# Kernel tuning notes

Measured on AMD Instinct MI355X. Metric: run time of the kernel, lower is better.

Reference implementation:

```python
import jax, jax.numpy as jnp
import numpy as np

ALPHA = 0.2          # LeakyReLU negative slope
NEG = -9e15          # masking value from the torch source


def _gat_multihead(x, adj, W, a):
    """All nheads GATLayers (concat=True math, elu applied by caller).
    x: [B,N,F], adj: [B,N,N], W: [H,F,O], a: [H,2O]. Returns [B,H,N,O].
    Note a_input @ a decomposes as h_i.a[:O] + h_j.a[O:], so we never
    materialize the O(N^2 * 2O) pairwise concat tensor."""
    h = jnp.einsum('bnf,hfo->bhno', x, W)            # [B,H,N,O]
    O = h.shape[-1]
    s1 = jnp.einsum('bhno,ho->bhn', h, a[:, :O])     # h_i . a_src
    s2 = jnp.einsum('bhno,ho->bhn', h, a[:, O:])     # h_j . a_dst
    e = jax.nn.leaky_relu(s1[..., :, None] + s2[..., None, :], ALPHA)  # [B,H,N,N]
    att = jax.nn.softmax(jnp.where(adj[:, None] > 0, e, NEG), axis=-1)
    return jnp.einsum('bhij,bhjo->bhio', att, h)


def _gat_single(x, adj, W, a):
    """out_att GATLayer (concat=False, no elu). W: [F,O], a: [2O]."""
    h = jnp.einsum('bnf,fo->bno', x, W)
    O = W.shape[-1]
    s1 = h @ a[:O]
    s2 = h @ a[O:]
    e = jax.nn.leaky_relu(s1[:, :, None] + s2[:, None, :], ALPHA)
    att = jax.nn.softmax(jnp.where(adj > 0, e, NEG), axis=-1)
    return jnp.einsum('bij,bjo->bio', att, h)


def setup_inputs() -> dict:
    key = jax.random.key(0)
    ks = jax.random.split(key, 10)
    B, N, F = 2, 2048, 768
    H, O = 8, 256
    x = jax.random.normal(ks[0], (B, N, F), dtype=jnp.float32)
    # sparse-ish binary adjacency (adj>0 is all that matters) + self loops
    adj = (jax.random.uniform(ks[1], (B, N, N)) < 0.05).astype(jnp.float32)
    adj = jnp.maximum(adj, jnp.eye(N, dtype=jnp.float32)[None])
    mask = jnp.ones((B, N, 1), dtype=jnp.float32)  # unused by GAT.forward
    s = 0.05
    W_heads = jax.random.normal(ks[2], (H, F, O), dtype=jnp.float32) * s
    a_heads = jax.random.normal(ks[3], (H, 2 * O), dtype=jnp.float32) * s
    W_out = jax.random.normal(ks[4], (H * O, O), dtype=jnp.float32) * s
    a_out = jax.random.normal(ks[5], (2 * O,), dtype=jnp.float32) * s
    W_lin = jax.random.normal(ks[6], (O, H * O), dtype=jnp.float32) * s  # nn.Linear weight [out,in]
    b_lin = jnp.zeros((O,), dtype=jnp.float32)
    W_ln = jax.random.normal(ks[7], (O, O), dtype=jnp.float32) * s
    b_ln = jnp.zeros((O,), dtype=jnp.float32)
    return {"x": x, "adj": adj, "mask": mask, "W_heads": W_heads,
            "a_heads": a_heads, "W_out": W_out, "a_out": a_out,
            "W_lin": W_lin, "b_lin": b_lin, "W_ln": W_ln, "b_ln": b_ln}


def reference(x, adj, mask, W_heads, a_heads, W_out, a_out, W_lin, b_lin, W_ln, b_ln):
    # layer 0: multi-head GAT, elu, concat over heads (dropout=0 in eval)
    hp = jax.nn.elu(_gat_multihead(x, adj, W_heads, a_heads))  # [B,H,N,O]
    B, H, N, O = hp.shape
    x1 = jnp.transpose(hp, (0, 2, 1, 3)).reshape(B, N, H * O)
    # layer 1: residual linear + out_att (concat=False)
    x2 = x1 @ W_lin.T + b_lin + _gat_single(x1, adj, W_out, a_out)
    # final: relu(ln(x))
    return jax.nn.relu(x2 @ W_ln.T + b_ln)
```

## Files before the change

kernel.cpp:

```cpp
#include <hip/hip_runtime.h>
#include <hip/hip_bf16.h>

constexpr int Bb = 2, Nn = 2048, Ff = 768, Hh = 8, Oo = 256;

typedef __attribute__((ext_vector_type(8)))  short   short8;
typedef __attribute__((ext_vector_type(16))) float   f32x16;
typedef __attribute__((ext_vector_type(4)))  unsigned short ushort4_t;

__device__ inline unsigned short f2bf(float f) {
    unsigned u = __float_as_uint(f);
    u = (u + 0x7FFFu + ((u >> 16) & 1u)) >> 16;
    return (unsigned short)u;
}

__device__ inline void wfrag_kn_body(
        const float* __restrict__ W, unsigned short* __restrict__ out,
        int K, int N, int fblk, int t) {
    int f = fblk * 4 + (t >> 6);
    int slot = t & 63, kh = slot >> 5, lm = slot & 31;
    int nfk = K >> 4;
    int nt = f / nfk, kt = f - nt * nfk;
    const float* wp = W + (size_t)(kt * 16 + kh * 8) * N + nt * 32 + lm;
    ushort4_t o0, o1;
    o0.x = f2bf(wp[0]);             o0.y = f2bf(wp[(size_t)N]);
    o0.z = f2bf(wp[2 * (size_t)N]); o0.w = f2bf(wp[3 * (size_t)N]);
    o1.x = f2bf(wp[4 * (size_t)N]); o1.y = f2bf(wp[5 * (size_t)N]);
    o1.z = f2bf(wp[6 * (size_t)N]); o1.w = f2bf(wp[7 * (size_t)N]);
    unsigned short* op = out + (size_t)f * 512 + slot * 8;
    *(ushort4_t*)op = o0;
    *(ushort4_t*)(op + 4) = o1;
}

__device__ inline void wfrag_nk_body(
        const float* __restrict__ W, unsigned short* __restrict__ out,
        int K, int fblk, int t) {
    int f = fblk * 4 + (t >> 6);
    int slot = t & 63, kh = slot >> 5, lm = slot & 31;
    int nfk = K >> 4;
    int nt = f / nfk, kt = f - nt * nfk;
    const float* wp = W + (size_t)(nt * 32 + lm) * K + kt * 16 + kh * 8;
    float4 a = *(const float4*)wp, b = *(const float4*)(wp + 4);
    ushort4_t o0, o1;
    o0.x = f2bf(a.x); o0.y = f2bf(a.y); o0.z = f2bf(a.z); o0.w = f2bf(a.w);
    o1.x = f2bf(b.x); o1.y = f2bf(b.y); o1.z = f2bf(b.z); o1.w = f2bf(b.w);
    unsigned short* op = out + (size_t)f * 512 + slot * 8;
    *(ushort4_t*)op = o0;
    *(ushort4_t*)(op + 4) = o1;
}

__global__ __launch_bounds__(256) void prep_misc_kernel(
        const float* __restrict__ adj, unsigned long long* __restrict__ bits,
        const float* __restrict__ x, unsigned short* __restrict__ x_bf,
        const float* __restrict__ W_heads, unsigned short* __restrict__ WhF,
        const float* __restrict__ W_out,   unsigned short* __restrict__ WoF,
        const float* __restrict__ W_lin,   unsigned short* __restrict__ WlF,
        const float* __restrict__ W_ln,    unsigned short* __restrict__ WnF) {
    int blk = blockIdx.x, t = threadIdx.x;
    if (blk < 32768) {
        size_t gid = (size_t)blk * 256 + t;
        float v = adj[gid];
        unsigned long long m = __ballot(v > 0.f);
        if ((t & 63) == 0) bits[gid >> 6] = m;
    } else if (blk < 35840) {
        size_t i = (size_t)(blk - 32768) * 256 + t;
        float4 v = ((const float4*)x)[i];
        ushort4_t o;
        o.x = f2bf(v.x); o.y = f2bf(v.y); o.z = f2bf(v.z); o.w = f2bf(v.w);
        ((ushort4_t*)x_bf)[i] = o;
    } else if (blk < 36608) {
        int idx = blk - 35840;
        int head = idx / 96, fblk = idx - head * 96;
        wfrag_kn_body(W_heads + (size_t)head * Ff * Oo, WhF + (size_t)head * 384 * 512,
                      Ff, Oo, fblk, t);
    } else if (blk < 36864) {
        wfrag_kn_body(W_out, WoF, Hh * Oo, Oo, blk - 36608, t);
    } else if (blk < 37120) {
        wfrag_nk_body(W_lin, WlF, Hh * Oo, blk - 36864, t);
    } else {
        wfrag_nk_body(W_ln, WnF, Oo, blk - 37120, t);
    }
}

template<int SWAPZ>
__global__ __launch_bounds__(256) void gemm32_kernel(
        const unsigned short* __restrict__ A, int K, long long sA, int bAshift,
        const unsigned short* __restrict__ BF, long long sB, int bmask,
        float* __restrict__ C, long long sC,
        unsigned short* __restrict__ CF, long long sCF, int Mtot,
        const float* __restrict__ bias, int mode,
        const float* __restrict__ aall, int amask,
        float* __restrict__ E1p, float* __restrict__ E1n, float2* __restrict__ E2pn) {
    int z  = SWAPZ ? blockIdx.x : blockIdx.z;
    int mx = SWAPZ ? blockIdx.y : blockIdx.x;
    A  += (size_t)(z >> bAshift) * sA;
    BF += (size_t)(z & bmask) * sB;
    if (C) C += (size_t)z * sC;
    if (CF) CF += (size_t)z * sCF;
    int m0 = mx * 32;
    int t = threadIdx.x;
    int wv = t >> 6, lane = t & 63;
    int lm = lane & 31, kh = lane >> 5;
    int nfk = K >> 4;
    __shared__ __align__(16) unsigned short As[32][136];
    f32x16 acc[2] = {};
    int sr = t >> 3, sc2 = (t & 7) * 16;
    const unsigned short* ag  = A + (size_t)(m0 + sr) * K + sc2;
    const unsigned short* bg0 = BF + (size_t)(wv * 2) * nfk * 512;
    const unsigned short* bg1 = bg0 + (size_t)nfk * 512;
    for (int k0 = 0; k0 < K; k0 += 128) {
        *(short8*)&As[sr][sc2]     = *(const short8*)(ag + k0);
        *(short8*)&As[sr][sc2 + 8] = *(const short8*)(ag + k0 + 8);
        int kt0 = k0 >> 4;
        __syncthreads();
#pragma unroll
        for (int s = 0; s < 8; ++s) {
            short8 a0 = *(const short8*)&As[lm][s * 16 + kh * 8];
            short8 b0 = *(const short8*)(bg0 + (size_t)(kt0 + s) * 512 + lane * 8);
            short8 b1 = *(const short8*)(bg1 + (size_t)(kt0 + s) * 512 + lane * 8);
            acc[0] = __builtin_amdgcn_mfma_f32_32x32x16_bf16(a0, b0, acc[0], 0, 0, 0);
            acc[1] = __builtin_amdgcn_mfma_f32_32x32x16_bf16(a0, b1, acc[1], 0, 0, 0);
        }
        __syncthreads();
    }
#pragma unroll
    for (int nt = 0; nt < 2; ++nt) {
        int colg = wv * 64 + nt * 32 + lm;
        float bv = (mode == 2) ? bias[colg] : 0.f;
        if (C) {
#pragma unroll
            for (int reg = 0; reg < 16; ++reg) {
                int rl = 4 * kh + (reg & 3) + 8 * (reg >> 2);
                float v = acc[nt][reg];
                if (mode == 2) { v += bv; v = fmaxf(v, 0.f); }
                C[(size_t)(m0 + rl) * 256 + colg] = v;
            }
        }
        if (mode == 1) {
#pragma unroll
            for (int q = 0; q < 4; ++q) {
                int kt = m0 / 16 + (q >> 1);
                size_t fi = ((size_t)(colg >> 5) * (Mtot / 16) + kt) * 512 +
                            ((q & 1) * 32 + (colg & 31)) * 8 + kh * 4;
                ushort4_t pk;
                pk.x = f2bf(acc[nt][q * 4 + 0]);
                pk.y = f2bf(acc[nt][q * 4 + 1]);
                pk.z = f2bf(acc[nt][q * 4 + 2]);
                pk.w = f2bf(acc[nt][q * 4 + 3]);
                *(ushort4_t*)(CF + fi) = pk;
            }
        }
    }
    if (aall) {
        const float* av = aall + (size_t)(z & amask) * 512;
        float a1v0 = av[wv * 64 + lm],       a1v1 = av[wv * 64 + 32 + lm];
        float a2v0 = av[256 + wv * 64 + lm], a2v1 = av[256 + wv * 64 + 32 + lm];
        float* sbuf = (float*)As;
#pragma unroll
        for (int reg = 0; reg < 16; ++reg) {
            int rl = 4 * kh + (reg & 3) + 8 * (reg >> 2);
            float v1 = acc[0][reg] * a1v0 + acc[1][reg] * a1v1;
            float v2 = acc[0][reg] * a2v0 + acc[1][reg] * a2v1;
#pragma unroll
            for (int m = 1; m <= 16; m <<= 1) {
                v1 += __shfl_xor(v1, m, 64);
                v2 += __shfl_xor(v2, m, 64);
            }
            if (lm == 0) { sbuf[rl * 8 + wv] = v1; sbuf[rl * 8 + 4 + wv] = v2; }
        }
        __syncthreads();
        if (t < 32) {
            float s1 = sbuf[t * 8] + sbuf[t * 8 + 1] + sbuf[t * 8 + 2] + sbuf[t * 8 + 3];
            float s2 = sbuf[t * 8 + 4] + sbuf[t * 8 + 5] + sbuf[t * 8 + 6] + sbuf[t * 8 + 7];
            size_t ei = (size_t)z * Nn + m0 + t;
            E1p[ei] = __expf(s1);
            E1n[ei] = __expf(0.2f * s1);
            E2pn[ei] = make_float2(__expf(s2), __expf(0.2f * s2));
        }
    }
}

__global__ __launch_bounds__(512) void gemm32_dual_kernel(
        const unsigned short* __restrict__ A, int K, long long sA,
        const unsigned short* __restrict__ BF,
        unsigned short* __restrict__ h2f, float* __restrict__ lin,
        const float* __restrict__ a_out,
        float* __restrict__ E1p, float* __restrict__ E1n, float2* __restrict__ E2pn) {
    int b = blockIdx.z, ng = blockIdx.y;
    A += (size_t)b * sA;
    int nfk = K >> 4;
    BF += (size_t)ng * 8 * nfk * 512;
    int m0 = blockIdx.x * 32;
    int t = threadIdx.x;
    int wv = t >> 6, lane = t & 63;
    int lm = lane & 31, kh = lane >> 5;
    __shared__ __align__(16) unsigned short As[32][136];
    f32x16 acc = {};
    int sr = t >> 4, sc2 = (t & 15) * 8;
    const unsigned short* ag = A + (size_t)(m0 + sr) * K + sc2;
    const unsigned short* bg = BF + (size_t)wv * nfk * 512;
    for (int k0 = 0; k0 < K; k0 += 128) {
        *(short8*)&As[sr][sc2] = *(const short8*)(ag + k0);
        int kt0 = k0 >> 4;
        __syncthreads();
#pragma unroll
        for (int s = 0; s < 8; ++s) {
            short8 a0 = *(const short8*)&As[lm][s * 16 + kh * 8];
            short8 b0 = *(const short8*)(bg + (size_t)(kt0 + s) * 512 + lane * 8);
            acc = __builtin_amdgcn_mfma_f32_32x32x16_bf16(a0, b0, acc, 0, 0, 0);
        }
        __syncthreads();
    }
    int colg = wv * 32 + lm;
    if (ng == 1) {
        float* C = lin + (size_t)b * Nn * 256;
#pragma unroll
        for (int reg = 0; reg < 16; ++reg) {
            int rl = 4 * kh + (reg & 3) + 8 * (reg >> 2);
            C[(size_t)(m0 + rl) * 256 + colg] = acc[reg];
        }
    } else {
        unsigned short* CF = h2f + (size_t)b * 524288;
#pragma unroll
        for (int q = 0; q < 4; ++q) {
            int kt = m0 / 16 + (q >> 1);
            size_t fi = ((size_t)(colg >> 5) * 128 + kt) * 512 +
                        ((q & 1) * 32 + (colg & 31)) * 8 + kh * 4;
            ushort4_t pk;
            pk.x = f2bf(acc[q * 4 + 0]);
            pk.y = f2bf(acc[q * 4 + 1]);
            pk.z = f2bf(acc[q * 4 + 2]);
            pk.w = f2bf(acc[q * 4 + 3]);
            *(ushort4_t*)(CF + fi) = pk;
        }
        float a1v = a_out[colg];
        float a2v = a_out[256 + colg];
        float* sbuf = (float*)As;
#pragma unroll
        for (int reg = 0; reg < 16; ++reg) {
            int rl = 4 * kh + (reg & 3) + 8 * (reg >> 2);
            float v1 = acc[reg] * a1v;
            float v2 = acc[reg] * a2v;
#pragma unroll
            for (int m = 1; m <= 16; m <<= 1) {
                v1 += __shfl_xor(v1, m, 64);
                v2 += __shfl_xor(v2, m, 64);
            }
            if (lm == 0) { sbuf[rl * 16 + wv] = v1; sbuf[rl * 16 + 8 + wv] = v2; }
        }
        __syncthreads();
        if (t < 32) {
            float s1 = 0.f, s2 = 0.f;
#pragma unroll
            for (int k = 0; k < 8; ++k) {
                s1 += sbuf[t * 16 + k];
                s2 += sbuf[t * 16 + 8 + k];
            }
            size_t ei = (size_t)b * Nn + m0 + t;
            E1p[ei] = __expf(s1);
            E1n[ei] = __expf(0.2f * s1);
            E2pn[ei] = make_float2(__expf(s2), __expf(0.2f * s2));
        }
    }
}

__global__ __launch_bounds__(256) void gemm32_final_kernel(
        const float* __restrict__ pacc, const float* __restrict__ plsum,
        const float* __restrict__ lin, const float* __restrict__ b_lin,
        const unsigned short* __restrict__ BF, const float* __restrict__ b_ln,
        float* __restrict__ out) {
    int b = blockIdx.z, oc = blockIdx.y;
    int m0 = blockIdx.x * 32;
    int t = threadIdx.x;
    int wv = t >> 6, lane = t & 63;
    int lm = lane & 31, kh = lane >> 5;
    constexpr int nfk = 16;
    __shared__ __align__(16) unsigned short As[32][136];
    f32x16 acc = {};
    int sr = t >> 3, sc2 = (t & 7) * 16;
    int row = m0 + sr;
    int BN = Bb * Nn;
    size_t prow = (size_t)b * Nn + row;
    float li = 1.f / (plsum[prow] + plsum[prow + BN] + plsum[prow + 2 * BN] + plsum[prow + 3 * BN]);
    size_t ps4 = (size_t)Bb * Nn * 256;
    const unsigned short* bg = BF + (size_t)(oc * 4 + wv) * nfk * 512;
    for (int k0 = 0; k0 < 256; k0 += 128) {
        int o = k0 + sc2;
        size_t pidx = prow * 256 + o;
#pragma unroll
        for (int g = 0; g < 4; ++g) {
            float4 s4 = *(const float4*)(pacc + pidx + 4 * g);
#pragma unroll
            for (int k = 1; k < 4; ++k) {
                float4 q = *(const float4*)(pacc + k * ps4 + pidx + 4 * g);
                s4.x += q.x; s4.y += q.y; s4.z += q.z; s4.w += q.w;
            }
            float4 lv = *(const float4*)(lin + pidx + 4 * g);
            float4 bv = *(const float4*)(b_lin + o + 4 * g);
            ushort4_t pk;
            pk.x = f2bf(s4.x * li + lv.x + bv.x);
            pk.y = f2bf(s4.y * li + lv.y + bv.y);
            pk.z = f2bf(s4.z * li + lv.z + bv.z);
            pk.w = f2bf(s4.w * li + lv.w + bv.w);
            *(ushort4_t*)&As[sr][sc2 + 4 * g] = pk;
        }
        int kt0 = k0 >> 4;
        __syncthreads();
#pragma unroll
        for (int s = 0; s < 8; ++s) {
            short8 a0 = *(const short8*)&As[lm][s * 16 + kh * 8];
            short8 b0 = *(const short8*)(bg + (size_t)(kt0 + s) * 512 + lane * 8);
            acc = __builtin_amdgcn_mfma_f32_32x32x16_bf16(a0, b0, acc, 0, 0, 0);
        }
        __syncthreads();
    }
    float* C = out + (size_t)b * Nn * 256;
    int colg = oc * 128 + wv * 32 + lm;
    float bv = b_ln[colg];
#pragma unroll
    for (int reg = 0; reg < 16; ++reg) {
        int rl = 4 * kh + (reg & 3) + 8 * (reg >> 2);
        float v = fmaxf(acc[reg] + bv, 0.f);
        C[(size_t)(m0 + rl) * 256 + colg] = v;
    }
}

template<int JLEN, int MODE, int SWAPXY>
__global__ __launch_bounds__(256, 4) void attn_v8_kernel(
        const unsigned short* __restrict__ hfrag,
        const unsigned* __restrict__ bits,
        const float* __restrict__ E1p, const float* __restrict__ E1n,
        const float2* __restrict__ E2pn,
        unsigned short* __restrict__ outbf, int ldo,
        float* __restrict__ pacc, float* __restrict__ plsum,
        int hshift) {
    constexpr int W = JLEN / 32, NC = JLEN / 64, ABS = W + 1;
    int it = SWAPXY ? blockIdx.y : blockIdx.x;
    int bh = SWAPXY ? blockIdx.x : blockIdx.y;
    int js = blockIdx.z;
    int b = bh >> hshift, hd = bh & ((1 << hshift) - 1);
    int i0 = it * 32, jbase = js * JLEN;
    int kt0 = js * (JLEN / 16);
    int t = threadIdx.x, lane = t & 63;
    int wv = t >> 6, lm = lane & 31, kh = lane >> 5;
    int ti = t & 31, jq = t >> 5;

    __shared__ unsigned ab[32 * ABS];
    __shared__ __align__(16) unsigned short ps[2][32][64];
    __shared__ float lred[32][9];
    __shared__ float linv[32];

    const unsigned* bb = bits + ((size_t)b * Nn + i0) * 64 + (jbase >> 5);
    for (int k = t; k < 32 * W; k += 256) {
        int r = k / W, w0 = k - r * W;
        ab[r * ABS + w0] = bb[(size_t)r * 64 + w0];
    }
    __syncthreads();

    float e1p = E1p[(size_t)bh * Nn + i0 + ti];
    float e1n = E1n[(size_t)bh * Nn + i0 + ti];
    const float4* e2base = (const float4*)(E2pn + (size_t)bh * Nn + jbase);

    const unsigned short* bg0 = hfrag + (size_t)bh * 524288 + (size_t)(wv * 2) * 128 * 512;
    const unsigned short* bg1 = bg0 + 128 * 512;

    f32x16 acc[2] = {};
    float lp0 = 0.f, lp1 = 0.f;
    short8 Bpp[4][2];

    auto loadBs = [&](int c, int s, int slot) {
        int kt = kt0 + c * 4 + s;
        Bpp[slot][0] = *(const short8*)(bg0 + (size_t)kt * 512 + lane * 8);
        Bpp[slot][1] = *(const short8*)(bg1 + (size_t)kt * 512 + lane * 8);
    };
    auto computeP = [&](int c, int buf) {
        int cj = c * 64;
        unsigned word = ab[ti * ABS + (cj >> 5) + (jq >> 2)];
        unsigned field = (word >> ((jq & 3) * 8)) & 0xffu;
        const float4* ep = e2base + ((cj + jq * 8) >> 1);
        unsigned pk[4];
#pragma unroll
        for (int u = 0; u < 4; ++u) {
            float4 q = ep[u];
            float p0 = fmaxf(e1p * q.x, e1n * q.y);
            p0 = ((field >> (2 * u)) & 1u) ? p0 : 0.f;
            float p1 = fmaxf(e1p * q.z, e1n * q.w);
            p1 = ((field >> (2 * u + 1)) & 1u) ? p1 : 0.f;
            if (u & 1) lp1 += p0 + p1; else lp0 += p0 + p1;
            __hip_bfloat162 hv = __float22bfloat162_rn(make_float2(p0, p1));
            pk[u] = *(unsigned*)&hv;
        }
        uint4 v; v.x = pk[0]; v.y = pk[1]; v.z = pk[2]; v.w = pk[3];
        *(uint4*)&ps[buf][ti][(jq ^ (ti & 7)) * 8] = v;
    };
    auto mfmaS = [&](int buf, int s, int slot) {
        int g = 2 * s + kh;
        short8 a0 = *(const short8*)&ps[buf][lm][(g ^ (lm & 7)) * 8];
        __builtin_amdgcn_s_setprio(1);
        acc[0] = __builtin_amdgcn_mfma_f32_32x32x16_bf16(a0, Bpp[slot][0], acc[0], 0, 0, 0);
        acc[1] = __builtin_amdgcn_mfma_f32_32x32x16_bf16(a0, Bpp[slot][1], acc[1], 0, 0, 0);
        __builtin_amdgcn_s_setprio(0);
    };

    computeP(0, 0);
    loadBs(0, 0, 0); loadBs(0, 1, 1); loadBs(0, 2, 2); loadBs(0, 3, 3);
    __syncthreads();
    for (int c = 0; c + 1 < NC; ++c) {
        int cb = c & 1, nb = cb ^ 1;
        computeP(c + 1, nb);
        mfmaS(cb, 0, 0);  loadBs(c + 1, 0, 0);
        mfmaS(cb, 1, 1);  loadBs(c + 1, 1, 1);
        mfmaS(cb, 2, 2);  loadBs(c + 1, 2, 2);
        mfmaS(cb, 3, 3);  loadBs(c + 1, 3, 3);
        __syncthreads();
    }
    {
        int cb = (NC - 1) & 1;
        mfmaS(cb, 0, 0);
        mfmaS(cb, 1, 1);
        mfmaS(cb, 2, 2);
        mfmaS(cb, 3, 3);
    }

    lred[ti][jq] = lp0 + lp1;
    __syncthreads();
    if (MODE == 0) {
        if (t < 32) {
            float s = 0.f;
#pragma unroll
            for (int k = 0; k < 8; ++k) s += lred[t][k];
            linv[t] = 1.f / s;
        }
        __syncthreads();
#pragma unroll
        for (int nt = 0; nt < 2; ++nt) {
            int o = wv * 64 + nt * 32 + lm;
#pragma unroll
            for (int reg = 0; reg < 16; ++reg) {
                int rl = 4 * kh + (reg & 3) + 8 * (reg >> 2);
                float v = acc[nt][reg] * linv[rl];
                v = v > 0.f ? v : expm1f(v);
                outbf[((size_t)b * Nn + i0 + rl) * ldo + (size_t)hd * Oo + o] = f2bf(v);
            }
        }
    } else {
        if (t < 32) {
            float s = 0.f;
#pragma unroll
            for (int k = 0; k < 8; ++k) s += lred[t][k];
            plsum[((size_t)js * Bb + b) * Nn + i0 + t] = s;
        }
        float* pa = pacc + (((size_t)js * Bb + b) * Nn) * 256;
#pragma unroll
        for (int nt = 0; nt < 2; ++nt) {
            int o = wv * 64 + nt * 32 + lm;
#pragma unroll
            for (int reg = 0; reg < 16; ++reg) {
                int rl = 4 * kh + (reg & 3) + 8 * (reg >> 2);
                pa[(size_t)(i0 + rl) * 256 + o] = acc[nt][reg];
            }
        }
    }
}

extern "C" void kernel_launch(void* const* d_in, const int* in_sizes, int n_in,
                              void* d_out, int out_size, void* d_ws, size_t ws_size,
                              hipStream_t stream) {
    const float* x       = (const float*)d_in[0];
    const float* adj     = (const float*)d_in[1];
    const float* W_heads = (const float*)d_in[3];
    const float* a_heads = (const float*)d_in[4];
    const float* W_out   = (const float*)d_in[5];
    const float* a_out   = (const float*)d_in[6];
    const float* W_lin   = (const float*)d_in[7];
    const float* b_lin   = (const float*)d_in[8];
    const float* W_ln    = (const float*)d_in[9];
    const float* b_ln    = (const float*)d_in[10];

    char* w = (char*)d_ws;
    float* pacc     = (float*)(w);
    float* lin      = (float*)(w + 33554432);
    float* E1p_mh   = (float*)(w + 41943040);
    float* E1n_mh   = (float*)(w + 42074112);
    float2* E2pn_mh = (float2*)(w + 42205184);
    float* E1p_sh   = (float*)(w + 42467328);
    float* E1n_sh   = (float*)(w + 42483712);
    float2* E2pn_sh = (float2*)(w + 42500096);
    unsigned long long* bits = (unsigned long long*)(w + 42532864);
    unsigned short* x_bf  = (unsigned short*)(w + 43581440);
    unsigned short* WhF   = (unsigned short*)(w + 49872896);
    unsigned short* WoF   = (unsigned short*)(w + 53018624);
    unsigned short* WlF   = (unsigned short*)(w + 54067200);
    unsigned short* WnF   = (unsigned short*)(w + 55115776);
    unsigned short* hfrag = (unsigned short*)(w + 55246848);
    unsigned short* h2frag= (unsigned short*)(w + 72024064);
    unsigned short* x1_bf = (unsigned short*)(w + 74121216);
    float* plsum = E1p_mh;

    prep_misc_kernel<<<37152, 256, 0, stream>>>(
        adj, bits, x, x_bf, W_heads, WhF, W_out, WoF, W_lin, WlF, W_ln, WnF);

    gemm32_kernel<1><<<dim3(Bb * Hh, Nn / 32, 1), 256, 0, stream>>>(
        x_bf, Ff, (long long)Nn * Ff, 3, WhF, 384LL * 512, 7,
        nullptr, 0, hfrag, 524288, Nn, nullptr, 1,
        a_heads, 7, E1p_mh, E1n_mh, E2pn_mh);
    attn_v8_kernel<2048, 0, 1><<<dim3(Bb * Hh, Nn / 32, 1), 256, 0, stream>>>(
        hfrag, (const unsigned*)bits, E1p_mh, E1n_mh, E2pn_mh,
        x1_bf, Hh * Oo, nullptr, nullptr, 3);
    gemm32_dual_kernel<<<dim3(Nn / 32, 2, Bb), 512, 0, stream>>>(
        x1_bf, Hh * Oo, (long long)Nn * Hh * Oo, WoF, h2frag, lin,
        a_out, E1p_sh, E1n_sh, E2pn_sh);
    attn_v8_kernel<512, 1, 0><<<dim3(Nn / 32, Bb, 4), 256, 0, stream>>>(
        h2frag, (const unsigned*)bits, E1p_sh, E1n_sh, E2pn_sh,
        nullptr, 0, pacc, plsum, 0);
    gemm32_final_kernel<<<dim3(Nn / 32, 2, Bb), 256, 0, stream>>>(
        pacc, plsum, lin, b_lin, WnF, b_ln, (float*)d_out);
}
```

Measured before the change: 248.0 us.

## Restructure attention kernel to split K across waves with register-resident P fragments

The attention kernel now has each wave own a slice of the neighbour (K) dimension and compute all 256 output columns for it. Before, waves split the output columns and shared a P tile staged through double-buffered LDS. Each wave builds its P fragment directly in registers as the MFMA B-operand, which removes the per-chunk LDS round trip and the block barriers in the main loop. The partial sums from the four waves are combined through a 64KB LDS reduction in the epilogue, which then writes vectorised stores. The cost is eight accumulator tiles per wave, more registers, launch bounds lowered to 2 blocks per SIMD, and a larger LDS footprint that reduces occupancy.

```diff
diff --git a/kernel.cpp b/kernel.cpp
--- a/kernel.cpp
+++ b/kernel.cpp
@@ -325,7 +325,7 @@
 }
 
 template<int JLEN, int MODE, int SWAPXY>
-__global__ __launch_bounds__(256, 4) void attn_v8_kernel(
+__global__ __launch_bounds__(256, 2) void attn_v10_kernel(
         const unsigned short* __restrict__ hfrag,
         const unsigned* __restrict__ bits,
         const float* __restrict__ E1p, const float* __restrict__ E1n,
@@ -333,130 +333,137 @@
         unsigned short* __restrict__ outbf, int ldo,
         float* __restrict__ pacc, float* __restrict__ plsum,
         int hshift) {
-    constexpr int W = JLEN / 32, NC = JLEN / 64, ABS = W + 1;
+    constexpr int W = JLEN / 32;
+    constexpr int NC = JLEN / 64;
     int it = SWAPXY ? blockIdx.y : blockIdx.x;
     int bh = SWAPXY ? blockIdx.x : blockIdx.y;
     int js = blockIdx.z;
     int b = bh >> hshift, hd = bh & ((1 << hshift) - 1);
     int i0 = it * 32, jbase = js * JLEN;
     int kt0 = js * (JLEN / 16);
-    int t = threadIdx.x, lane = t & 63;
-    int wv = t >> 6, lm = lane & 31, kh = lane >> 5;
-    int ti = t & 31, jq = t >> 5;
-
-    __shared__ unsigned ab[32 * ABS];
-    __shared__ __align__(16) unsigned short ps[2][32][64];
-    __shared__ float lred[32][9];
-    __shared__ float linv[32];
+    int t = threadIdx.x;
+    int wv = t >> 6, lane = t & 63;
+    int lm = lane & 31, kh = lane >> 5;
+    int jq = wv * 2 + kh;
+
+    __shared__ __align__(16) char smem[65536 + 512];
+    float4*   epi4 = (float4*)smem;
+    unsigned* ab   = (unsigned*)smem;
+    float*    lred = (float*)(smem + 65536);
 
     const unsigned* bb = bits + ((size_t)b * Nn + i0) * 64 + (jbase >> 5);
     for (int k = t; k < 32 * W; k += 256) {
         int r = k / W, w0 = k - r * W;
-        ab[r * ABS + w0] = bb[(size_t)r * 64 + w0];
+        ab[r * W + w0] = bb[(size_t)r * 64 + w0];
     }
     __syncthreads();
 
-    float e1p = E1p[(size_t)bh * Nn + i0 + ti];
-    float e1n = E1n[(size_t)bh * Nn + i0 + ti];
+    float e1p = E1p[(size_t)bh * Nn + i0 + lm];
+    float e1n = E1n[(size_t)bh * Nn + i0 + lm];
     const float4* e2base = (const float4*)(E2pn + (size_t)bh * Nn + jbase);
-
-    const unsigned short* bg0 = hfrag + (size_t)bh * 524288 + (size_t)(wv * 2) * 128 * 512;
-    const unsigned short* bg1 = bg0 + 128 * 512;
-
-    f32x16 acc[2] = {};
+    const unsigned short* ag = hfrag + (size_t)bh * 524288 + lane * 8;
+
+    f32x16 acc[8] = {};
+    short8 A[8];
+    float4 e2a[4], e2b[4];
     float lp0 = 0.f, lp1 = 0.f;
-    short8 Bpp[4][2];
-
-    auto loadBs = [&](int c, int s, int slot) {
-        int kt = kt0 + c * 4 + s;
-        Bpp[slot][0] = *(const short8*)(bg0 + (size_t)kt * 512 + lane * 8);
-        Bpp[slot][1] = *(const short8*)(bg1 + (size_t)kt * 512 + lane * 8);
+
+    auto loadA = [&](int cn, int mt) {
+        int kt = kt0 + cn * 4 + wv;
+        A[mt] = *(const short8*)(ag + ((size_t)mt * 128 + kt) * 512);
     };
-    auto computeP = [&](int c, int buf) {
-        int cj = c * 64;
-        unsigned word = ab[ti * ABS + (cj >> 5) + (jq >> 2)];
+    auto loadE2 = [&](int cn, float4 (&buf)[4]) {
+        const float4* ep = e2base + ((cn * 64 + jq * 8) >> 1);
+#pragma unroll
+        for (int u = 0; u < 4; ++u) buf[u] = ep[u];
+    };
+    auto computeP = [&](int c, const float4 (&buf)[4], short8& pbo) {
+        unsigned word = ab[lm * W + c * 2 + (jq >> 2)];
         unsigned field = (word >> ((jq & 3) * 8)) & 0xffu;
-        const float4* ep = e2base + ((cj + jq * 8) >> 1);
-        unsigned pk[4];
+        union { unsigned u[4]; short8 s; } pk;
 #pragma unroll
         for (int u = 0; u < 4; ++u) {
-            float4 q = ep[u];
+            float4 q = buf[u];
             float p0 = fmaxf(e1p * q.x, e1n * q.y);
             p0 = ((field >> (2 * u)) & 1u) ? p0 : 0.f;
             float p1 = fmaxf(e1p * q.z, e1n * q.w);
             p1 = ((field >> (2 * u + 1)) & 1u) ? p1 : 0.f;
-            if (u & 1) lp1 += p0 + p1; else lp0 += p0 + p1;
+            lp0 += p0; lp1 += p1;
             __hip_bfloat162 hv = __float22bfloat162_rn(make_float2(p0, p1));
-            pk[u] = *(unsigned*)&hv;
-        }
-        uint4 v; v.x = pk[0]; v.y = pk[1]; v.z = pk[2]; v.w = pk[3];
-        *(uint4*)&ps[buf][ti][(jq ^ (ti & 7)) * 8] = v;
+            pk.u[u] = *(unsigned*)&hv;
+        }
+        pbo = pk.s;
     };
-    auto mfmaS = [&](int buf, int s, int slot) {
-        int g = 2 * s + kh;
-        short8 a0 = *(const short8*)&ps[buf][lm][(g ^ (lm & 7)) * 8];
+    auto mfma8 = [&](const short8& pb, int cn) {
         __builtin_amdgcn_s_setprio(1);
-        acc[0] = __builtin_amdgcn_mfma_f32_32x32x16_bf16(a0, Bpp[slot][0], acc[0], 0, 0, 0);
-        acc[1] = __builtin_amdgcn_mfma_f32_32x32x16_bf16(a0, Bpp[slot][1], acc[1], 0, 0, 0);
+#pragma unroll
+        for (int mt = 0; mt < 8; ++mt) {
+            acc[mt] = __builtin_amdgcn_mfma_f32_32x32x16_bf16(A[mt], pb, acc[mt], 0, 0, 0);
+            loadA(cn, mt);
+        }
         __builtin_amdgcn_s_setprio(0);
     };
 
-    computeP(0, 0);
-    loadBs(0, 0, 0); loadBs(0, 1, 1); loadBs(0, 2, 2); loadBs(0, 3, 3);
+    loadE2(0, e2a);
+#pragma unroll
+    for (int mt = 0; mt < 8; ++mt) loadA(0, mt);
+    short8 pb0, pb1;
+#pragma unroll 1
+    for (int c = 0; c < NC; c += 2) {
+        loadE2(c + 1, e2b);
+        computeP(c, e2a, pb0);
+        mfma8(pb0, c + 1);
+        loadE2(c + 2, e2a);
+        computeP(c + 1, e2b, pb1);
+        mfma8(pb1, c + 2);
+    }
+
+    lp0 += lp1;
+    lp0 += __shfl_xor(lp0, 32, 64);
+    if (lane < 32) lred[lm * 4 + wv] = lp0;
     __syncthreads();
-    for (int c = 0; c + 1 < NC; ++c) {
-        int cb = c & 1, nb = cb ^ 1;
-        computeP(c + 1, nb);
-        mfmaS(cb, 0, 0);  loadBs(c + 1, 0, 0);
-        mfmaS(cb, 1, 1);  loadBs(c + 1, 1, 1);
-        mfmaS(cb, 2, 2);  loadBs(c + 1, 2, 2);
-        mfmaS(cb, 3, 3);  loadBs(c + 1, 3, 3);
-        __syncthreads();
-    }
-    {
-        int cb = (NC - 1) & 1;
-        mfmaS(cb, 0, 0);
-        mfmaS(cb, 1, 1);
-        mfmaS(cb, 2, 2);
-        mfmaS(cb, 3, 3);
-    }
-
-    lred[ti][jq] = lp0 + lp1;
-    __syncthreads();
-    if (MODE == 0) {
-        if (t < 32) {
-            float s = 0.f;
-#pragma unroll
-            for (int k = 0; k < 8; ++k) s += lred[t][k];
-            linv[t] = 1.f / s;
-        }
-        __syncthreads();
-#pragma unroll
-        for (int nt = 0; nt < 2; ++nt) {
-            int o = wv * 64 + nt * 32 + lm;
-#pragma unroll
-            for (int reg = 0; reg < 16; ++reg) {
-                int rl = 4 * kh + (reg & 3) + 8 * (reg >> 2);
-                float v = acc[nt][reg] * linv[rl];
-                v = v > 0.f ? v : expm1f(v);
-                outbf[((size_t)b * Nn + i0 + rl) * ldo + (size_t)hd * Oo + o] = f2bf(v);
-            }
-        }
-    } else {
-        if (t < 32) {
-            float s = 0.f;
-#pragma unroll
-            for (int k = 0; k < 8; ++k) s += lred[t][k];
-            plsum[((size_t)js * Bb + b) * Nn + i0 + t] = s;
-        }
-        float* pa = pacc + (((size_t)js * Bb + b) * Nn) * 256;
-#pragma unroll
-        for (int nt = 0; nt < 2; ++nt) {
-            int o = wv * 64 + nt * 32 + lm;
-#pragma unroll
-            for (int reg = 0; reg < 16; ++reg) {
-                int rl = 4 * kh + (reg & 3) + 8 * (reg >> 2);
-                pa[(size_t)(i0 + rl) * 256 + o] = acc[nt][reg];
+    float rs = lred[lm * 4 + 0] + lred[lm * 4 + 1] + lred[lm * 4 + 2] + lred[lm * 4 + 3];
+    float fi = 1.f / rs;
+    if (MODE == 1 && t < 32)
+        plsum[((size_t)js * Bb + b) * Nn + i0 + t] = rs;
+
+    size_t obase = (MODE == 0)
+        ? ((size_t)b * Nn + i0 + lm) * ldo + (size_t)hd * Oo
+        : (((size_t)js * Bb + b) * Nn + i0 + lm) * 256;
+#pragma unroll
+    for (int r = 0; r < 2; ++r) {
+        if (r) __syncthreads();
+#pragma unroll
+        for (int q = 0; q < 4; ++q)
+#pragma unroll
+            for (int g = 0; g < 4; ++g)
+                epi4[((wv * 4 + q) * 4 + g) * 64 + lane] =
+                    make_float4(acc[r * 4 + q][4 * g], acc[r * 4 + q][4 * g + 1],
+                                acc[r * 4 + q][4 * g + 2], acc[r * 4 + q][4 * g + 3]);
+        __syncthreads();
+        int mt = r * 4 + wv;
+#pragma unroll
+        for (int g = 0; g < 4; ++g) {
+            float4 s0 = epi4[(0 * 16 + wv * 4 + g) * 64 + lane];
+            float4 s1 = epi4[(1 * 16 + wv * 4 + g) * 64 + lane];
+            float4 s2 = epi4[(2 * 16 + wv * 4 + g) * 64 + lane];
+            float4 s3 = epi4[(3 * 16 + wv * 4 + g) * 64 + lane];
+            float v0 = s0.x + s1.x + s2.x + s3.x;
+            float v1 = s0.y + s1.y + s2.y + s3.y;
+            float v2 = s0.z + s1.z + s2.z + s3.z;
+            float v3 = s0.w + s1.w + s2.w + s3.w;
+            int ob = mt * 32 + 8 * g + 4 * kh;
+            if (MODE == 0) {
+                v0 *= fi; v1 *= fi; v2 *= fi; v3 *= fi;
+                v0 = v0 > 0.f ? v0 : expm1f(v0);
+                v1 = v1 > 0.f ? v1 : expm1f(v1);
+                v2 = v2 > 0.f ? v2 : expm1f(v2);
+                v3 = v3 > 0.f ? v3 : expm1f(v3);
+                ushort4_t pk4;
+                pk4.x = f2bf(v0); pk4.y = f2bf(v1); pk4.z = f2bf(v2); pk4.w = f2bf(v3);
+                *(ushort4_t*)&outbf[obase + ob] = pk4;
+            } else {
+                *(float4*)&pacc[obase + ob] = make_float4(v0, v1, v2, v3);
             }
         }
     }
@@ -503,13 +510,13 @@
         x_bf, Ff, (long long)Nn * Ff, 3, WhF, 384LL * 512, 7,
         nullptr, 0, hfrag, 524288, Nn, nullptr, 1,
         a_heads, 7, E1p_mh, E1n_mh, E2pn_mh);
-    attn_v8_kernel<2048, 0, 1><<<dim3(Bb * Hh, Nn / 32, 1), 256, 0, stream>>>(
+    attn_v10_kernel<2048, 0, 1><<<dim3(Bb * Hh, Nn / 32, 1), 256, 0, stream>>>(
         hfrag, (const unsigned*)bits, E1p_mh, E1n_mh, E2pn_mh,
         x1_bf, Hh * Oo, nullptr, nullptr, 3);
     gemm32_dual_kernel<<<dim3(Nn / 32, 2, Bb), 512, 0, stream>>>(
         x1_bf, Hh * Oo, (long long)Nn * Hh * Oo, WoF, h2frag, lin,
         a_out, E1p_sh, E1n_sh, E2pn_sh);
-    attn_v8_kernel<512, 1, 0><<<dim3(Nn / 32, Bb, 4), 256, 0, stream>>>(
+    attn_v10_kernel<512, 1, 0><<<dim3(Nn / 32, Bb, 4), 256, 0, stream>>>(
         h2frag, (const unsigned*)bits, E1p_sh, E1n_sh, E2pn_sh,
         nullptr, 0, pacc, plsum, 0);
     gemm32_final_kernel<<<dim3(Nn / 32, 2, Bb), 256, 0, stream>>>(
```

New measurement: 333.7 us. 1.35x slower.

## Use 64-row query tiles in multi-head attention kernel to reuse hfrag loads

Applied to the files above, without the earlier changes.

Adds an attention kernel variant that processes 64 query rows per block instead of 32, so each loaded B fragment of h feeds four MFMAs (two row halves × two column tiles) instead of two. This halves global/L2 traffic for the value matrix and E2 loads per output row in the multi-head layer. The cost is more accumulator registers (launch bounds lowered to 2 blocks/SM) and half as many blocks, reducing occupancy and parallelism. The single-head layer keeps the renamed 32-row kernel.

```diff
diff --git a/kernel.cpp b/kernel.cpp
--- a/kernel.cpp
+++ b/kernel.cpp
@@ -325,7 +325,7 @@
 }
 
 template<int JLEN, int MODE, int SWAPXY>
-__global__ __launch_bounds__(256, 4) void attn_v8_kernel(
+__global__ __launch_bounds__(256, 4) void attn32_kernel(
         const unsigned short* __restrict__ hfrag,
         const unsigned* __restrict__ bits,
         const float* __restrict__ E1p, const float* __restrict__ E1n,
@@ -457,6 +457,172 @@
             for (int reg = 0; reg < 16; ++reg) {
                 int rl = 4 * kh + (reg & 3) + 8 * (reg >> 2);
                 pa[(size_t)(i0 + rl) * 256 + o] = acc[nt][reg];
+            }
+        }
+    }
+}
+
+template<int JLEN, int MODE, int SWAPXY>
+__global__ __launch_bounds__(256, 2) void attn64_kernel(
+        const unsigned short* __restrict__ hfrag,
+        const unsigned* __restrict__ bits,
+        const float* __restrict__ E1p, const float* __restrict__ E1n,
+        const float2* __restrict__ E2pn,
+        unsigned short* __restrict__ outbf, int ldo,
+        float* __restrict__ pacc, float* __restrict__ plsum,
+        int hshift) {
+    constexpr int W = JLEN / 32, NC = JLEN / 64, ABS = W + 1;
+    int it = SWAPXY ? blockIdx.y : blockIdx.x;
+    int bh = SWAPXY ? blockIdx.x : blockIdx.y;
+    int js = blockIdx.z;
+    int b = bh >> hshift, hd = bh & ((1 << hshift) - 1);
+    int i0 = it * 64, jbase = js * JLEN;
+    int kt0 = js * (JLEN / 16);
+    int t = threadIdx.x, lane = t & 63;
+    int wv = t >> 6, lm = lane & 31, kh = lane >> 5;
+    int ti = t & 31, jq = t >> 5;
+
+    __shared__ unsigned ab[64 * ABS];
+    __shared__ __align__(16) unsigned short ps[2][64][64];
+    __shared__ float lred[64][9];
+    __shared__ float linv[64];
+
+    const unsigned* bb = bits + ((size_t)b * Nn + i0) * 64 + (jbase >> 5);
+    for (int k = t; k < 64 * W; k += 256) {
+        int r = k / W, w0 = k - r * W;
+        ab[r * ABS + w0] = bb[(size_t)r * 64 + w0];
+    }
+    __syncthreads();
+
+    float e1pA = E1p[(size_t)bh * Nn + i0 + ti];
+    float e1nA = E1n[(size_t)bh * Nn + i0 + ti];
+    float e1pB = E1p[(size_t)bh * Nn + i0 + 32 + ti];
+    float e1nB = E1n[(size_t)bh * Nn + i0 + 32 + ti];
+    const float4* e2base = (const float4*)(E2pn + (size_t)bh * Nn + jbase);
+
+    const unsigned short* bg0 = hfrag + (size_t)bh * 524288 + (size_t)(wv * 2) * 128 * 512;
+    const unsigned short* bg1 = bg0 + 128 * 512;
+
+    f32x16 acc[4] = {};
+    float lpA = 0.f, lpB = 0.f;
+    short8 Bpp[4][2];
+
+    auto loadBs = [&](int c, int s, int slot) {
+        int kt = kt0 + c * 4 + s;
+        Bpp[slot][0] = *(const short8*)(bg0 + (size_t)kt * 512 + lane * 8);
+        Bpp[slot][1] = *(const short8*)(bg1 + (size_t)kt * 512 + lane * 8);
+    };
+    auto computeP = [&](int c, int buf) {
+        int cj = c * 64;
+        int wi = (cj >> 5) + (jq >> 2);
+        unsigned wordA = ab[ti * ABS + wi];
+        unsigned wordB = ab[(ti + 32) * ABS + wi];
+        unsigned fieldA = (wordA >> ((jq & 3) * 8)) & 0xffu;
+        unsigned fieldB = (wordB >> ((jq & 3) * 8)) & 0xffu;
+        const float4* ep = e2base + ((cj + jq * 8) >> 1);
+        unsigned pkA[4], pkB[4];
+#pragma unroll
+        for (int u = 0; u < 4; ++u) {
+            float4 q = ep[u];
+            float a0v = fmaxf(e1pA * q.x, e1nA * q.y);
+            a0v = ((fieldA >> (2 * u)) & 1u) ? a0v : 0.f;
+            float a1v = fmaxf(e1pA * q.z, e1nA * q.w);
+            a1v = ((fieldA >> (2 * u + 1)) & 1u) ? a1v : 0.f;
+            lpA += a0v + a1v;
+            float b0v = fmaxf(e1pB * q.x, e1nB * q.y);
+            b0v = ((fieldB >> (2 * u)) & 1u) ? b0v : 0.f;
+            float b1v = fmaxf(e1pB * q.z, e1nB * q.w);
+            b1v = ((fieldB >> (2 * u + 1)) & 1u) ? b1v : 0.f;
+            lpB += b0v + b1v;
+            __hip_bfloat162 hA = __float22bfloat162_rn(make_float2(a0v, a1v));
+            __hip_bfloat162 hB = __float22bfloat162_rn(make_float2(b0v, b1v));
+            pkA[u] = *(unsigned*)&hA;
+            pkB[u] = *(unsigned*)&hB;
+        }
+        int col = (jq ^ (ti & 7)) * 8;
+        uint4 vA; vA.x = pkA[0]; vA.y = pkA[1]; vA.z = pkA[2]; vA.w = pkA[3];
+        uint4 vB; vB.x = pkB[0]; vB.y = pkB[1]; vB.z = pkB[2]; vB.w = pkB[3];
+        *(uint4*)&ps[buf][ti][col] = vA;
+        *(uint4*)&ps[buf][ti + 32][col] = vB;
+    };
+    auto mfmaS = [&](int buf, int s, int slot) {
+        int g = 2 * s + kh;
+        int col = (g ^ (lm & 7)) * 8;
+        short8 a0 = *(const short8*)&ps[buf][lm][col];
+        short8 a1 = *(const short8*)&ps[buf][32 + lm][col];
+        __builtin_amdgcn_s_setprio(1);
+        acc[0] = __builtin_amdgcn_mfma_f32_32x32x16_bf16(a0, Bpp[slot][0], acc[0], 0, 0, 0);
+        acc[1] = __builtin_amdgcn_mfma_f32_32x32x16_bf16(a0, Bpp[slot][1], acc[1], 0, 0, 0);
+        acc[2] = __builtin_amdgcn_mfma_f32_32x32x16_bf16(a1, Bpp[slot][0], acc[2], 0, 0, 0);
+        acc[3] = __builtin_amdgcn_mfma_f32_32x32x16_bf16(a1, Bpp[slot][1], acc[3], 0, 0, 0);
+        __builtin_amdgcn_s_setprio(0);
+    };
+
+    computeP(0, 0);
+    loadBs(0, 0, 0); loadBs(0, 1, 1); loadBs(0, 2, 2); loadBs(0, 3, 3);
+    __syncthreads();
+    for (int c = 0; c + 1 < NC; ++c) {
+        int cb = c & 1, nb = cb ^ 1;
+        computeP(c + 1, nb);
+        mfmaS(cb, 0, 0);  loadBs(c + 1, 0, 0);
+        mfmaS(cb, 1, 1);  loadBs(c + 1, 1, 1);
+        mfmaS(cb, 2, 2);  loadBs(c + 1, 2, 2);
+        mfmaS(cb, 3, 3);  loadBs(c + 1, 3, 3);
+        __syncthreads();
+    }
+    {
+        int cb = (NC - 1) & 1;
+        mfmaS(cb, 0, 0);
+        mfmaS(cb, 1, 1);
+        mfmaS(cb, 2, 2);
+        mfmaS(cb, 3, 3);
+    }
+
+    lred[ti][jq] = lpA;
+    lred[ti + 32][jq] = lpB;
+    __syncthreads();
+    if (MODE == 0) {
+        if (t < 64) {
+            float s = 0.f;
+#pragma unroll
+            for (int k = 0; k < 8; ++k) s += lred[t][k];
+            linv[t] = 1.f / s;
+        }
+        __syncthreads();
+#pragma unroll
+        for (int ih = 0; ih < 2; ++ih) {
+#pragma unroll
+            for (int nt = 0; nt < 2; ++nt) {
+                int o = wv * 64 + nt * 32 + lm;
+#pragma unroll
+                for (int reg = 0; reg < 16; ++reg) {
+                    int rl = 4 * kh + (reg & 3) + 8 * (reg >> 2);
+                    int row = ih * 32 + rl;
+                    float v = acc[ih * 2 + nt][reg] * linv[row];
+                    v = v > 0.f ? v : expm1f(v);
+                    outbf[((size_t)b * Nn + i0 + row) * ldo + (size_t)hd * Oo + o] = f2bf(v);
+                }
+            }
+        }
+    } else {
+        if (t < 64) {
+            float s = 0.f;
+#pragma unroll
+            for (int k = 0; k < 8; ++k) s += lred[t][k];
+            plsum[((size_t)js * Bb + b) * Nn + i0 + t] = s;
+        }
+        float* pa = pacc + (((size_t)js * Bb + b) * Nn) * 256;
+#pragma unroll
+        for (int ih = 0; ih < 2; ++ih) {
+#pragma unroll
+            for (int nt = 0; nt < 2; ++nt) {
+                int o = wv * 64 + nt * 32 + lm;
+#pragma unroll
+                for (int reg = 0; reg < 16; ++reg) {
+                    int rl = 4 * kh + (reg & 3) + 8 * (reg >> 2);
+                    int row = ih * 32 + rl;
+                    pa[(size_t)(i0 + row) * 256 + o] = acc[ih * 2 + nt][reg];
+                }
             }
         }
     }
@@ -503,13 +669,13 @@
         x_bf, Ff, (long long)Nn * Ff, 3, WhF, 384LL * 512, 7,
         nullptr, 0, hfrag, 524288, Nn, nullptr, 1,
         a_heads, 7, E1p_mh, E1n_mh, E2pn_mh);
-    attn_v8_kernel<2048, 0, 1><<<dim3(Bb * Hh, Nn / 32, 1), 256, 0, stream>>>(
+    attn64_kernel<2048, 0, 1><<<dim3(Bb * Hh, Nn / 64, 1), 256, 0, stream>>>(
         hfrag, (const unsigned*)bits, E1p_mh, E1n_mh, E2pn_mh,
         x1_bf, Hh * Oo, nullptr, nullptr, 3);
     gemm32_dual_kernel<<<dim3(Nn / 32, 2, Bb), 512, 0, stream>>>(
         x1_bf, Hh * Oo, (long long)Nn * Hh * Oo, WoF, h2frag, lin,
         a_out, E1p_sh, E1n_sh, E2pn_sh);
-    attn_v8_kernel<512, 1, 0><<<dim3(Nn / 32, Bb, 4), 256, 0, stream>>>(
+    attn32_kernel<512, 1, 0><<<dim3(Nn / 32, Bb, 4), 256, 0, stream>>>(
         h2frag, (const unsigned*)bits, E1p_sh, E1n_sh, E2pn_sh,
         nullptr, 0, pacc, plsum, 0);
     gemm32_final_kernel<<<dim3(Nn / 32, 2, Bb), 256, 0, stream>>>(
```

Result: faster. 237.0 us (median of 3 runs) (-4.4%).
